# Performance work log

Hardware: AMD Instinct MI355X
Metric: run time of the kernel (lower is better)

The kernel has to match this reference:

```python
import jax, jax.numpy as jnp
import numpy as np

N_NODES = 100000
D = 128
N_ETYPES = 4
E_PER_TYPE = 400000


def setup_inputs() -> dict:
    key = jax.random.key(0)
    k_h, k_src, k_dst, k_w = jax.random.split(key, 4)
    h = jax.random.normal(k_h, (N_NODES, D), dtype=jnp.float32)
    src = jax.random.randint(k_src, (N_ETYPES, E_PER_TYPE), 0, N_NODES, dtype=jnp.int32)
    dst = jax.random.randint(k_dst, (N_ETYPES, E_PER_TYPE), 0, N_NODES, dtype=jnp.int32)
    # Linear(2*D, 1) with xavier_uniform init
    bound = float(np.sqrt(6.0 / (2 * D + 1)))
    W_weight = jax.random.uniform(k_w, (1, 2 * D), dtype=jnp.float32,
                                  minval=-bound, maxval=bound)
    W_bias = jnp.zeros((1,), dtype=jnp.float32)
    return {"h": h, "src": src, "dst": dst, "W_weight": W_weight, "W_bias": W_bias}


def reference(h, src, dst, W_weight, W_bias):
    # Per edge type: gather src/dst node feats, concat, shared Linear(2D->1), sigmoid.
    # cat([h_u, h_v]) @ W.T == h_u @ Wu.T + h_v @ Wv.T (avoids materializing the concat).
    d = h.shape[1]
    Wu = W_weight[:, :d]   # [1, D]
    Wv = W_weight[:, d:]   # [1, D]
    h_u = h[src]           # [T, E, D] gather (irregular access)
    h_v = h[dst]           # [T, E, D]
    score = jnp.einsum('ted,od->teo', h_u, Wu) \
          + jnp.einsum('ted,od->teo', h_v, Wv) + W_bias  # [T, E, 1]
    s = jax.nn.sigmoid(score)
    # scores dict entries are the per-etype slices s[t]; s_l = concat over etypes
    return s.reshape(-1, 1)
```

## Files before the change

kernel.cpp:

```cpp
#include <hip/hip_runtime.h>
#include <math.h>

#define NODES   100000
#define DIM     128
#define NEDGES  1600000
#define NQUADS  (NEDGES / 4)
#define NGROUPS (NODES / 8)

#define LOG2E 1.44269504088896340736f

typedef int   v4i __attribute__((ext_vector_type(4)));
typedef float v4f __attribute__((ext_vector_type(4)));

__device__ __forceinline__ float fast_sigmoid(float x) {
    return __builtin_amdgcn_rcpf(1.0f + __builtin_amdgcn_exp2f(-x * LOG2E));
}

__device__ __forceinline__ float dot4(v4f a, v4f b) {
    return a.x * b.x + a.y * b.y + a.z * b.z + a.w * b.w;
}

__global__ __launch_bounds__(256) void node_proj_kernel(
    const float* __restrict__ h,
    const float* __restrict__ W,
    const float* __restrict__ bias_ptr,
    float* __restrict__ pu,
    float* __restrict__ pv)
{
    const int tid  = blockIdx.x * 256 + threadIdx.x;
    const int lane = tid & 31;
    const int grp  = tid >> 5;
    if (grp >= NGROUPS) return;
    const int n0 = grp * 8;

    const v4f wu = *reinterpret_cast<const v4f*>(W + lane * 4);
    const v4f wv = *reinterpret_cast<const v4f*>(W + DIM + lane * 4);
    const float b = bias_ptr[0];

    const float* hb = h + (size_t)n0 * DIM + lane * 4;
    v4f hr[8];
    #pragma unroll
    for (int j = 0; j < 8; ++j)
        hr[j] = *reinterpret_cast<const v4f*>(hb + j * DIM);

    float su[8], sv[8];
    #pragma unroll
    for (int j = 0; j < 8; ++j) {
        su[j] = dot4(hr[j], wu);
        sv[j] = dot4(hr[j], wv);
    }

    #pragma unroll
    for (int off = 16; off >= 1; off >>= 1) {
        #pragma unroll
        for (int j = 0; j < 8; ++j) {
            su[j] += __shfl_xor(su[j], off);
            sv[j] += __shfl_xor(sv[j], off);
        }
    }

    if (lane == 0) {
        v4f a0 = { su[0], su[1], su[2], su[3] };
        v4f a1 = { su[4], su[5], su[6], su[7] };
        v4f b0 = { sv[0] + b, sv[1] + b, sv[2] + b, sv[3] + b };
        v4f b1 = { sv[4] + b, sv[5] + b, sv[6] + b, sv[7] + b };
        *reinterpret_cast<v4f*>(pu + n0)     = a0;
        *reinterpret_cast<v4f*>(pu + n0 + 4) = a1;
        *reinterpret_cast<v4f*>(pv + n0)     = b0;
        *reinterpret_cast<v4f*>(pv + n0 + 4) = b1;
    }
}

__global__ __launch_bounds__(256) void edge_score_kernel(
    const int*   __restrict__ src,
    const int*   __restrict__ dst,
    const float* __restrict__ pu,
    const float* __restrict__ pv,
    float* __restrict__ out)
{
    int i = blockIdx.x * 256 + threadIdx.x;
    if (i >= NQUADS) return;

    v4i s4 = reinterpret_cast<const v4i*>(src)[i];
    v4i d4 = reinterpret_cast<const v4i*>(dst)[i];

    float a0 = pu[s4.x], b0 = pv[d4.x];
    float a1 = pu[s4.y], b1 = pv[d4.y];
    float a2 = pu[s4.z], b2 = pv[d4.z];
    float a3 = pu[s4.w], b3 = pv[d4.w];

    v4f r;
    r.x = fast_sigmoid(a0 + b0);
    r.y = fast_sigmoid(a1 + b1);
    r.z = fast_sigmoid(a2 + b2);
    r.w = fast_sigmoid(a3 + b3);

    __builtin_nontemporal_store(r, reinterpret_cast<v4f*>(out) + i);
}

extern "C" void kernel_launch(void* const* d_in, const int* in_sizes, int n_in,
                              void* d_out, int out_size, void* d_ws, size_t ws_size,
                              hipStream_t stream) {
    const float* h    = (const float*)d_in[0];
    const int*   src  = (const int*)d_in[1];
    const int*   dst  = (const int*)d_in[2];
    const float* W    = (const float*)d_in[3];
    const float* bias = (const float*)d_in[4];
    float* out = (float*)d_out;

    float* pu = (float*)d_ws;
    float* pv = pu + NODES;

    node_proj_kernel<<<(NGROUPS * 32 + 255) / 256, 256, 0, stream>>>(h, W, bias, pu, pv);

    edge_score_kernel<<<(NQUADS + 255) / 256, 256, 0, stream>>>(src, dst, pu, pv, out);
}
```

Before: 31.69 us.

## Pack per-node projections as fp16 pairs and process one edge per thread

Node projections pu and pv+bias are now packed into a single 32-bit word of two fp16 values with round-toward-zero conversion, halving the projection table to 400KB. The aim is to keep it resident in cache for the random gathers. The edge kernel now handles one edge per thread with scalar loads instead of four edges per thread with vector loads, which launches four times as many threads. Using fp16 adds rounding error to the scores before the sigmoid, and scalar index loads may cost more instruction overhead.

```diff
diff --git a/kernel.cpp b/kernel.cpp
--- a/kernel.cpp
+++ b/kernel.cpp
@@ -4,13 +4,14 @@
 #define NODES   100000
 #define DIM     128
 #define NEDGES  1600000
-#define NQUADS  (NEDGES / 4)
 #define NGROUPS (NODES / 8)
 
 #define LOG2E 1.44269504088896340736f
 
-typedef int   v4i __attribute__((ext_vector_type(4)));
-typedef float v4f __attribute__((ext_vector_type(4)));
+typedef int      v4i  __attribute__((ext_vector_type(4)));
+typedef uint32_t v4u  __attribute__((ext_vector_type(4)));
+typedef float    v4f  __attribute__((ext_vector_type(4)));
+typedef _Float16 h2   __attribute__((ext_vector_type(2)));
 
 __device__ __forceinline__ float fast_sigmoid(float x) {
     return __builtin_amdgcn_rcpf(1.0f + __builtin_amdgcn_exp2f(-x * LOG2E));
@@ -24,8 +25,7 @@
     const float* __restrict__ h,
     const float* __restrict__ W,
     const float* __restrict__ bias_ptr,
-    float* __restrict__ pu,
-    float* __restrict__ pv)
+    uint32_t* __restrict__ p)
 {
     const int tid  = blockIdx.x * 256 + threadIdx.x;
     const int lane = tid & 31;
@@ -60,42 +60,37 @@
     }
 
     if (lane == 0) {
-        v4f a0 = { su[0], su[1], su[2], su[3] };
-        v4f a1 = { su[4], su[5], su[6], su[7] };
-        v4f b0 = { sv[0] + b, sv[1] + b, sv[2] + b, sv[3] + b };
-        v4f b1 = { sv[4] + b, sv[5] + b, sv[6] + b, sv[7] + b };
-        *reinterpret_cast<v4f*>(pu + n0)     = a0;
-        *reinterpret_cast<v4f*>(pu + n0 + 4) = a1;
-        *reinterpret_cast<v4f*>(pv + n0)     = b0;
-        *reinterpret_cast<v4f*>(pv + n0 + 4) = b1;
+        uint32_t w[8];
+        #pragma unroll
+        for (int j = 0; j < 8; ++j) {
+            w[j] = __builtin_bit_cast(uint32_t,
+                       __builtin_amdgcn_cvt_pkrtz(su[j], sv[j] + b));
+        }
+        v4u w0 = { w[0], w[1], w[2], w[3] };
+        v4u w1 = { w[4], w[5], w[6], w[7] };
+        *reinterpret_cast<v4u*>(p + n0)     = w0;
+        *reinterpret_cast<v4u*>(p + n0 + 4) = w1;
     }
 }
 
 __global__ __launch_bounds__(256) void edge_score_kernel(
-    const int*   __restrict__ src,
-    const int*   __restrict__ dst,
-    const float* __restrict__ pu,
-    const float* __restrict__ pv,
+    const int*      __restrict__ src,
+    const int*      __restrict__ dst,
+    const uint32_t* __restrict__ p,
     float* __restrict__ out)
 {
-    int i = blockIdx.x * 256 + threadIdx.x;
-    if (i >= NQUADS) return;
+    const int i = blockIdx.x * 256 + threadIdx.x;
 
-    v4i s4 = reinterpret_cast<const v4i*>(src)[i];
-    v4i d4 = reinterpret_cast<const v4i*>(dst)[i];
+    const int s = src[i];
+    const int d = dst[i];
 
-    float a0 = pu[s4.x], b0 = pv[d4.x];
-    float a1 = pu[s4.y], b1 = pv[d4.y];
-    float a2 = pu[s4.z], b2 = pv[d4.z];
-    float a3 = pu[s4.w], b3 = pv[d4.w];
+    const uint32_t ws = p[s];
+    const uint32_t wd = p[d];
 
-    v4f r;
-    r.x = fast_sigmoid(a0 + b0);
-    r.y = fast_sigmoid(a1 + b1);
-    r.z = fast_sigmoid(a2 + b2);
-    r.w = fast_sigmoid(a3 + b3);
+    const float a = (float)__builtin_bit_cast(h2, ws).x;
+    const float c = (float)__builtin_bit_cast(h2, wd).y;
 
-    __builtin_nontemporal_store(r, reinterpret_cast<v4f*>(out) + i);
+    __builtin_nontemporal_store(fast_sigmoid(a + c), out + i);
 }
 
 extern "C" void kernel_launch(void* const* d_in, const int* in_sizes, int n_in,
@@ -108,10 +103,9 @@
     const float* bias = (const float*)d_in[4];
     float* out = (float*)d_out;
 
-    float* pu = (float*)d_ws;
-    float* pv = pu + NODES;
+    uint32_t* p = (uint32_t*)d_ws;
 
-    node_proj_kernel<<<(NGROUPS * 32 + 255) / 256, 256, 0, stream>>>(h, W, bias, pu, pv);
+    node_proj_kernel<<<(NGROUPS * 32 + 255) / 256, 256, 0, stream>>>(h, W, bias, p);
 
-    edge_score_kernel<<<(NQUADS + 255) / 256, 256, 0, stream>>>(src, dst, pu, pv, out);
+    edge_score_kernel<<<NEDGES / 256, 256, 0, stream>>>(src, dst, p, out);
 }
```

After: 29.56 us. 1.07x faster.
